# Kernel tuning notes

Measured on AMD Instinct MI355X. Metric: run time of the kernel, lower is better.

Reference implementation:

```python
import jax, jax.numpy as jnp
import numpy as np

B, N, K, C, H, W = 2, 8, 8, 256, 96, 96
CTX = C + K + 4 * K + 13  # 309
HID = 256
ALPHA = 0.3          # REFINE_EMA_ALPHA
TEMP = 1.0           # READOUT_TEMPERATURE
SIM_HIGH, SIM_LOW = 0.8, 0.3
A_KEEP, A_REFINE, A_REPLACE, A_SPAWN = 0, 1, 2, 3


def _l2norm(x, axis=-1, eps=1e-12):
    return x / jnp.maximum(jnp.linalg.norm(x, axis=axis, keepdims=True), eps)


def setup_inputs() -> dict:
    key = jax.random.key(0)
    ks = jax.random.split(key, 12)
    value = jax.random.normal(ks[0], (B, N, C, H, W), jnp.float32)
    frame_feat = jax.random.normal(ks[1], (B, C, H, W), jnp.float32)
    mask = jax.random.uniform(ks[2], (B, N, H, W), jnp.float32)
    proto = jax.random.normal(ks[3], (B, N, K, C), jnp.float32)
    age = jax.random.uniform(ks[4], (B, N, K), jnp.float32) * 10.0
    usage = jax.random.uniform(ks[5], (B, N, K), jnp.float32) * 5.0
    conf = jax.random.uniform(ks[6], (B, N, K), jnp.float32)
    valid = jax.random.randint(ks[7], (B, N, K), 0, 2).astype(bool)
    W1 = jax.random.normal(ks[8], (CTX, HID), jnp.float32) * 0.02
    b1 = jnp.zeros((HID,), jnp.float32)
    W2 = jax.random.normal(ks[9], (HID, 4), jnp.float32) * 0.02
    b2 = jnp.zeros((4,), jnp.float32)
    proto_gate = jnp.float32(1.0)
    frame_gate = jnp.float32(1.0)
    return dict(value=value, frame_feat=frame_feat, mask=mask, proto=proto,
                age=age, usage=usage, conf=conf, W1=W1, b1=b1, W2=W2, b2=b2,
                proto_gate=proto_gate, frame_gate=frame_gate, valid=valid)


def reference(value, frame_feat, mask, proto, age, usage, conf,
              W1, b1, W2, b2, proto_gate, frame_gate, valid):
    # ---- candidate prototype via masked pooling (PROTO_POOLING='mask') ----
    fv = value.reshape(B, N, C, H * W)                      # [B,N,C,HW]
    fm = mask.reshape(B, N, 1, H * W)                       # [B,N,1,HW]
    denom = jnp.maximum(fm.sum(-1), 1e-6)                   # [B,N,1]
    cand = (fv * fm).sum(-1) / denom                        # [B,N,C]
    mask_strength = fm.mean(-1)[..., 0]                     # [B,N]
    fallback = fv.mean(-1)
    cand = jnp.where((denom[..., 0] <= 1e-5)[..., None], fallback, cand)
    cand = _l2norm(cand)

    # ---- uncertainty features (prev_mask is None -> temporal term = 0) ----
    m = jnp.clip(mask, 1e-4, 1.0 - 1e-4)
    ent = -(m * jnp.log(m) + (1.0 - m) * jnp.log(1.0 - m))
    fg_prob = m.mean((-2, -1))
    fg_area = (m > 0.5).astype(jnp.float32).mean((-2, -1))
    gx = jnp.abs(m[..., 1:, :] - m[..., :-1, :]).mean((-2, -1))
    gy = jnp.abs(m[..., :, 1:] - m[..., :, :-1]).mean((-2, -1))
    unc = jnp.stack([ent.mean((-2, -1)), fg_prob, fg_area,
                     0.5 * (gx + gy), jnp.zeros_like(fg_prob)], -1)  # [B,N,5]

    # ---- context / similarity ----
    bank_n = _l2norm(proto)                                  # [B,N,K,C]
    sim = jnp.einsum('bnc,bnkc->bnk', cand, bank_n)
    sim = jnp.where(valid, sim, -1.0)
    g_t = jnp.broadcast_to(frame_feat.mean((2, 3))[:, None, :], (B, N, C))
    age_n = age / jnp.maximum(age.max(), 1.0)
    usage_n = usage / jnp.maximum(usage.max(), 1.0)
    bank_stats = jnp.stack([valid.astype(jnp.float32), age_n, usage_n, conf], -1)
    top2 = jax.lax.top_k(sim, 2)[0]
    t1, t2 = top2[..., 0], top2[..., 1]
    glob = jnp.stack([valid.astype(jnp.float32).mean(-1), age_n.max(-1),
                      usage_n.min(-1), conf.mean(-1), conf.max(-1)], -1)
    context = jnp.concatenate([g_t, sim, bank_stats.reshape(B, N, 4 * K),
                               jnp.stack([t1, t2, t1 - t2], -1), glob, unc], -1)
    logits = jax.nn.gelu(context @ W1 + b1, approximate=False) @ W2 + b2  # [B,N,4]

    any_valid = valid.any(-1)
    target_slot = jnp.where(any_valid, sim.argmax(-1), 0)
    max_sim = jnp.take_along_axis(sim, target_slot[..., None], -1)[..., 0]
    max_sim = jnp.where(any_valid, max_sim, -1.0)

    # ---- rule-based action selection ----
    action = jnp.where(~any_valid, A_SPAWN,
             jnp.where(max_sim >= SIM_HIGH, A_REFINE,
             jnp.where(max_sim >= SIM_LOW, A_KEEP, A_SPAWN)))

    # ---- victim / slot selection ----
    victim = (age_n + (1.0 - usage_n) + (1.0 - conf)).argmax(-1)
    first_empty = (~valid).argmax(-1)
    spawn_slot = jnp.where((~valid).any(-1), first_empty, victim)
    upd_slot = jnp.where(action == A_REFINE, target_slot, spawn_slot)

    # ---- policy-gated EMA scatter update of the bank ----
    onehot = jax.nn.one_hot(upd_slot, K, dtype=bool)                 # [B,N,K]
    refine_m = onehot & (action == A_REFINE)[..., None]
    write_m = onehot & (action == A_SPAWN)[..., None]
    refined = _l2norm((1.0 - ALPHA) * proto + ALPHA * cand[:, :, None, :])
    cand_b = jnp.broadcast_to(cand[:, :, None, :], proto.shape)
    proto_new = jnp.where(refine_m[..., None], refined,
                jnp.where(write_m[..., None], cand_b, proto))
    upd_m = refine_m | write_m
    age_new = jnp.where(upd_m, 0.0, age + 1.0)
    usage_new = usage + upd_m.astype(jnp.float32)
    conf_new = jnp.where(write_m, mask_strength[..., None],
               jnp.where(refine_m, jnp.maximum(conf, max_sim[..., None]), conf))
    valid_new = valid | write_m

    # ---- prototype-conditioned readout ----
    bank_nn = _l2norm(proto_new)                                      # [B,N,K,C]
    vn = value / jnp.maximum(jnp.linalg.norm(value, axis=2, keepdims=True), 1e-12)
    rsim = jnp.einsum('bnkc,bnchw->bnkhw', bank_nn, vn)
    rlog = jnp.where(valid_new[..., None, None], rsim / TEMP, -1e9)
    attn = jax.nn.softmax(rlog, axis=2)
    attn = attn * valid_new.any(-1)[..., None, None, None].astype(jnp.float32)
    proto_map = jnp.einsum('bnkhw,bnkc->bnchw', attn, proto_new)
    conditioned = value + proto_gate * proto_map + frame_gate * frame_feat[:, None]
    return conditioned
```

## Files before the change

### kernel.cpp

```cpp
#include <hip/hip_runtime.h>
#include <math.h>

constexpr int Bc = 2, Nc = 8, Kc = 8, Cc = 256, HWc = 96 * 96;
constexpr int BN = Bc * Nc;
constexpr int HW2 = HWc / 2;
constexpr float ALPHA = 0.3f;
constexpr float SIM_HIGH = 0.8f, SIM_LOW = 0.3f;
constexpr int TILES = 72;

__device__ __forceinline__ float wred_sum_all(float v) {
#pragma unroll
  for (int o = 32; o > 0; o >>= 1) v += __shfl_xor(v, o, 64);
  return v;
}
__device__ __forceinline__ float wred_sum(float v) {
#pragma unroll
  for (int o = 32; o > 0; o >>= 1) v += __shfl_down(v, o, 64);
  return v;
}
__device__ __forceinline__ float wred_max(float v) {
#pragma unroll
  for (int o = 32; o > 0; o >>= 1) v = fmaxf(v, __shfl_down(v, o, 64));
  return v;
}
__device__ __forceinline__ float bred_sum(float v, float* sc) {
  int lane = threadIdx.x & 63, wid = threadIdx.x >> 6;
  v = wred_sum(v);
  __syncthreads();
  if (lane == 0) sc[wid] = v;
  __syncthreads();
  return sc[0] + sc[1] + sc[2] + sc[3];
}
__device__ __forceinline__ float bred_max(float v, float* sc) {
  int lane = threadIdx.x & 63, wid = threadIdx.x >> 6;
  v = wred_max(v);
  __syncthreads();
  if (lane == 0) sc[wid] = v;
  __syncthreads();
  return fmaxf(fmaxf(sc[0], sc[1]), fmaxf(sc[2], sc[3]));
}

__device__ __forceinline__ float lane_bcast(float x, int c0) {
  return __int_as_float(__builtin_amdgcn_readlane(__float_as_int(x), c0));
}

__global__ __launch_bounds__(256) void k1_sums(const float* __restrict__ value,
                                               const float* __restrict__ mask,
                                               float* __restrict__ sum_v,
                                               float* __restrict__ sum_vm,
                                               float* __restrict__ msum) {
  const int bnc = blockIdx.x;
  const int bn = bnc >> 8;
  const int tid = threadIdx.x;
  const float4* v4 = (const float4*)(value + (size_t)bnc * HWc);
  const float4* m4 = (const float4*)(mask + (size_t)bn * HWc);
  float av = 0.f, avm = 0.f, am = 0.f;
#pragma unroll
  for (int i = 0; i < 9; ++i) {
    float4 v = v4[i * 256 + tid];
    float4 m = m4[i * 256 + tid];
    av += v.x + v.y + v.z + v.w;
    avm += v.x * m.x + v.y * m.y + v.z * m.z + v.w * m.w;
    am += (m.x + m.y) + (m.z + m.w);
  }
  __shared__ float sc[12];
  float rv = wred_sum(av);
  float rvm = wred_sum(avm);
  float rm = wred_sum(am);
  int lane = tid & 63, wid = tid >> 6;
  if (lane == 0) { sc[wid] = rv; sc[4 + wid] = rvm; sc[8 + wid] = rm; }
  __syncthreads();
  if (tid == 0) {
    sum_v[bnc] = sc[0] + sc[1] + sc[2] + sc[3];
    sum_vm[bnc] = sc[4] + sc[5] + sc[6] + sc[7];
    if ((bnc & 255) == 0)
      msum[bn] = sc[8] + sc[9] + sc[10] + sc[11];
  }
}

__global__ __launch_bounds__(256, 8) void k3_fused(
    const float* __restrict__ value, const float* __restrict__ frame,
    const float* __restrict__ mask_unused, const float* __restrict__ proto,
    const float* __restrict__ age, const float* __restrict__ usage,
    const float* __restrict__ conf, const int* __restrict__ valid,
    const float* __restrict__ sum_v, const float* __restrict__ sum_vm,
    const float* __restrict__ msum, const float* __restrict__ pgp,
    const float* __restrict__ fgp, float* __restrict__ out) {
  const int bn = blockIdx.x / TILES;
  const int tile = blockIdx.x % TILES;
  const int b = bn >> 3;
  const int tid = threadIdx.x;
  const int lane = tid & 63, w = tid >> 6;
  const int p2 = tile * 64 + lane;

  __shared__ union {
    struct { float cand[Cc]; float pn[Kc * Cc]; float sim[Kc]; } pre;
    float part[4 * 9 * 128];
  } u;
  __shared__ float sc[4];
  __shared__ float s_binv[Kc], s_vld[Kc];
  __shared__ int s_slot, s_ref, s_wr;

  float a = (tid < BN * Kc) ? age[tid] : -3e38f;
  float uu = (tid < BN * Kc) ? usage[tid] : -3e38f;
  const float age_den = fmaxf(bred_max(a, sc), 1.0f);
  const float usage_den = fmaxf(bred_max(uu, sc), 1.0f);

  const float denom = fmaxf(msum[bn], 1e-6f);

  const float sv = sum_v[bn * Cc + tid];
  const float svm = sum_vm[bn * Cc + tid];
  float cand = (denom <= 1e-5f) ? (sv * (1.0f / HWc)) : (svm / denom);
  const float css = bred_sum(cand * cand, sc);
  u.pre.cand[tid] = cand / fmaxf(sqrtf(css), 1e-12f);
  __syncthreads();

  const float4 c4 = ((const float4*)u.pre.cand)[lane];

  float4 p4k[2];
#pragma unroll
  for (int kk = 0; kk < 2; ++kk) {
    const int k = w + kk * 4;
    p4k[kk] = ((const float4*)(proto + ((size_t)bn * Kc + k) * Cc))[lane];
    const float4 p4 = p4k[kk];
    const float pss = wred_sum_all(p4.x * p4.x + p4.y * p4.y + p4.z * p4.z + p4.w * p4.w);
    const float pd  = wred_sum_all(p4.x * c4.x + p4.y * c4.y + p4.z * c4.z + p4.w * c4.w);
    if (lane == 0)
      u.pre.sim[k] = (valid[bn * Kc + k] != 0) ? (pd / fmaxf(sqrtf(pss), 1e-12f)) : -1.0f;
  }
  __syncthreads();

  if (tid == 0) {
    bool anyv = false;
    for (int k = 0; k < Kc; ++k) anyv = anyv || (valid[bn * Kc + k] != 0);
    int tslot = 0; float best = u.pre.sim[0];
    for (int k = 1; k < Kc; ++k)
      if (u.pre.sim[k] > best) { best = u.pre.sim[k]; tslot = k; }
    const float max_sim = anyv ? best : -1.0f;
    const int action = (!anyv) ? 3 : (max_sim >= SIM_HIGH ? 1 : (max_sim >= SIM_LOW ? 0 : 3));
    int victim = 0; float vb = -3e38f;
    for (int k = 0; k < Kc; ++k) {
      const float s = age[bn * Kc + k] / age_den + (1.f - usage[bn * Kc + k] / usage_den) +
                      (1.f - conf[bn * Kc + k]);
      if (s > vb) { vb = s; victim = k; }
    }
    int fe = 0; bool hasE = false;
    for (int k = 0; k < Kc; ++k)
      if (valid[bn * Kc + k] == 0) { fe = k; hasE = true; break; }
    const int spawn = hasE ? fe : victim;
    s_slot = (action == 1) ? tslot : spawn;
    s_ref = (action == 1);
    s_wr = (action == 3);
  }
  __syncthreads();

#pragma unroll
  for (int kk = 0; kk < 2; ++kk) {
    const int k = w + kk * 4;
    const float4 p4 = p4k[kk];
    float4 pn;
    if (k == s_slot && s_ref) {
      float4 t;
      t.x = (1.0f - ALPHA) * p4.x + ALPHA * c4.x;
      t.y = (1.0f - ALPHA) * p4.y + ALPHA * c4.y;
      t.z = (1.0f - ALPHA) * p4.z + ALPHA * c4.z;
      t.w = (1.0f - ALPHA) * p4.w + ALPHA * c4.w;
      const float tss = wred_sum_all(t.x * t.x + t.y * t.y + t.z * t.z + t.w * t.w);
      const float inv = 1.0f / fmaxf(sqrtf(tss), 1e-12f);
      pn.x = t.x * inv; pn.y = t.y * inv; pn.z = t.z * inv; pn.w = t.w * inv;
    } else if (k == s_slot && s_wr) {
      pn = c4;
    } else {
      pn = p4;
    }
    ((float4*)(u.pre.pn + k * Cc))[lane] = pn;
    const float bss = wred_sum_all(pn.x * pn.x + pn.y * pn.y + pn.z * pn.z + pn.w * pn.w);
    if (lane == 0) s_binv[k] = 1.0f / fmaxf(sqrtf(bss), 1e-12f);
  }
  if (tid < Kc)
    s_vld[tid] = ((valid[bn * Kc + tid] != 0) || (s_wr && tid == s_slot)) ? 1.0f : 0.0f;
  __syncthreads();

  float pnr[8], binv[8], vld[8];
#pragma unroll
  for (int k = 0; k < 8; ++k) {
    pnr[k] = u.pre.pn[k * Cc + w * 64 + lane];
    binv[k] = s_binv[k];
    vld[k] = s_vld[k];
  }
  __syncthreads();

  const float pg = pgp[0], fg = fgp[0];
  const float2* v2 = (const float2*)(value + (size_t)bn * Cc * HWc);
  const float2* f2 = (const float2*)(frame + (size_t)b * Cc * HWc);
  float2* o2 = (float2*)(out + (size_t)bn * Cc * HWc);

  float ss0 = 0.f, ss1 = 0.f;
  float d0[8], d1[8];
#pragma unroll
  for (int k = 0; k < 8; ++k) { d0[k] = 0.f; d1[k] = 0.f; }

#pragma unroll 8
  for (int c0 = 0; c0 < 64; ++c0) {
    const float2 v = v2[(size_t)(w * 64 + c0) * HW2 + p2];
    ss0 += v.x * v.x; ss1 += v.y * v.y;
#pragma unroll
    for (int k = 0; k < 8; ++k) {
      const float pk = lane_bcast(pnr[k], c0);
      d0[k] += pk * v.x;
      d1[k] += pk * v.y;
    }
  }

  float2* sp2 = (float2*)u.part;
#pragma unroll
  for (int k = 0; k < 8; ++k)
    sp2[(w * 9 + k) * 64 + lane] = make_float2(d0[k], d1[k]);
  sp2[(w * 9 + 8) * 64 + lane] = make_float2(ss0, ss1);
  __syncthreads();

  float a0[8], a1[8];
  {
    float dd0[9], dd1[9];
#pragma unroll
    for (int j = 0; j < 9; ++j) {
      const float2 t0 = sp2[(0 * 9 + j) * 64 + lane];
      const float2 t1 = sp2[(1 * 9 + j) * 64 + lane];
      const float2 t2 = sp2[(2 * 9 + j) * 64 + lane];
      const float2 t3 = sp2[(3 * 9 + j) * 64 + lane];
      dd0[j] = (t0.x + t1.x) + (t2.x + t3.x);
      dd1[j] = (t0.y + t1.y) + (t2.y + t3.y);
    }
    const float rn0 = 1.0f / fmaxf(sqrtf(dd0[8]), 1e-12f);
    const float rn1 = 1.0f / fmaxf(sqrtf(dd1[8]), 1e-12f);
    float m0 = -3e38f, m1 = -3e38f;
#pragma unroll
    for (int k = 0; k < 8; ++k) {
      const float scl = binv[k];
      dd0[k] *= scl * rn0;
      dd1[k] *= scl * rn1;
      if (vld[k] > 0.5f) { m0 = fmaxf(m0, dd0[k]); m1 = fmaxf(m1, dd1[k]); }
    }
    float sum0 = 0.f, sum1 = 0.f;
#pragma unroll
    for (int k = 0; k < 8; ++k) {
      a0[k] = (vld[k] > 0.5f) ? __expf(dd0[k] - m0) : 0.f;
      a1[k] = (vld[k] > 0.5f) ? __expf(dd1[k] - m1) : 0.f;
      sum0 += a0[k]; sum1 += a1[k];
    }
    const float i0 = (sum0 > 0.f) ? 1.0f / sum0 : 0.f;
    const float i1 = (sum1 > 0.f) ? 1.0f / sum1 : 0.f;
#pragma unroll
    for (int k = 0; k < 8; ++k) { a0[k] *= i0; a1[k] *= i1; }
  }

#pragma unroll 4
  for (int c0 = 0; c0 < 64; ++c0) {
    const size_t off = (size_t)(w * 64 + c0) * HW2 + p2;
    const float2 v = v2[off];
    const float2 f = f2[off];
    float pm0 = 0.f, pm1 = 0.f;
#pragma unroll
    for (int k = 0; k < 8; ++k) {
      const float pk = lane_bcast(pnr[k], c0);
      pm0 += a0[k] * pk;
      pm1 += a1[k] * pk;
    }
    float2 o;
    o.x = v.x + pg * pm0 + fg * f.x;
    o.y = v.y + pg * pm1 + fg * f.y;
    o2[off] = o;
  }
}

extern "C" void kernel_launch(void* const* d_in, const int* in_sizes, int n_in,
                              void* d_out, int out_size, void* d_ws, size_t ws_size,
                              hipStream_t stream) {
  const float* value = (const float*)d_in[0];
  const float* frame = (const float*)d_in[1];
  const float* mask  = (const float*)d_in[2];
  const float* proto = (const float*)d_in[3];
  const float* age   = (const float*)d_in[4];
  const float* usage = (const float*)d_in[5];
  const float* conf  = (const float*)d_in[6];
  const float* pg = (const float*)d_in[11];
  const float* fg = (const float*)d_in[12];
  const int* valid = (const int*)d_in[13];
  float* out = (float*)d_out;

  float* w = (float*)d_ws;
  float* sum_v  = w;
  float* sum_vm = w + 4096;
  float* msum   = w + 8192;

  hipLaunchKernelGGL(k1_sums, dim3(BN * Cc), dim3(256), 0, stream,
                     value, mask, sum_v, sum_vm, msum);
  hipLaunchKernelGGL(k3_fused, dim3(BN * TILES), dim3(256), 0, stream,
                     value, frame, mask, proto, age, usage, conf, valid,
                     sum_v, sum_vm, msum, pg, fg, out);
}
```

Baseline: 357.0 us.

## Split each wave across two channel halves and double tile count

Each wave now covers 32 pixel-pairs and splits its channel slice between two half-waves (even and odd channels), so the grid doubles from 72 to 144 tiles per (b,n). Channel-prototype broadcasts use __shfl instead of readlane, and partial dot products are combined across halves with a shfl_xor before the shared-memory reduction. The intent is more blocks and parallelism, shorter per-thread loops and smaller shared partials. The cost is that each block repeats the prototype-update preamble, shuffles go through LDS-style permutes rather than scalar readlane, and each memory access row is now 256 bytes rather than 512.

```diff
diff --git a/kernel.cpp b/kernel.cpp
--- a/kernel.cpp
+++ b/kernel.cpp
@@ -6,7 +6,7 @@
 constexpr int HW2 = HWc / 2;
 constexpr float ALPHA = 0.3f;
 constexpr float SIM_HIGH = 0.8f, SIM_LOW = 0.3f;
-constexpr int TILES = 72;
+constexpr int TILES = 144;
 
 __device__ __forceinline__ float wred_sum_all(float v) {
 #pragma unroll
@@ -38,10 +38,6 @@
   if (lane == 0) sc[wid] = v;
   __syncthreads();
   return fmaxf(fmaxf(sc[0], sc[1]), fmaxf(sc[2], sc[3]));
-}
-
-__device__ __forceinline__ float lane_bcast(float x, int c0) {
-  return __int_as_float(__builtin_amdgcn_readlane(__float_as_int(x), c0));
 }
 
 __global__ __launch_bounds__(256) void k1_sums(const float* __restrict__ value,
@@ -91,11 +87,14 @@
   const int b = bn >> 3;
   const int tid = threadIdx.x;
   const int lane = tid & 63, w = tid >> 6;
-  const int p2 = tile * 64 + lane;
+  const int h = lane >> 5;
+  const int p = lane & 31;
+  const int p2 = tile * 32 + p;
+  const int hbase = h << 5;
 
   __shared__ union {
     struct { float cand[Cc]; float pn[Kc * Cc]; float sim[Kc]; } pre;
-    float part[4 * 9 * 128];
+    float part[4 * 9 * 64];
   } u;
   __shared__ float sc[4];
   __shared__ float s_binv[Kc], s_vld[Kc];
@@ -181,10 +180,10 @@
     s_vld[tid] = ((valid[bn * Kc + tid] != 0) || (s_wr && tid == s_slot)) ? 1.0f : 0.0f;
   __syncthreads();
 
-  float pnr[8], binv[8], vld[8];
+  float rC[8], binv[8], vld[8];
 #pragma unroll
   for (int k = 0; k < 8; ++k) {
-    pnr[k] = u.pre.pn[k * Cc + w * 64 + lane];
+    rC[k] = u.pre.pn[k * Cc + w * 64 + 2 * p + h];
     binv[k] = s_binv[k];
     vld[k] = s_vld[k];
   }
@@ -201,22 +200,33 @@
   for (int k = 0; k < 8; ++k) { d0[k] = 0.f; d1[k] = 0.f; }
 
 #pragma unroll 8
-  for (int c0 = 0; c0 < 64; ++c0) {
-    const float2 v = v2[(size_t)(w * 64 + c0) * HW2 + p2];
+  for (int c0 = 0; c0 < 32; ++c0) {
+    const int c = w * 64 + 2 * c0 + h;
+    const float2 v = v2[(size_t)c * HW2 + p2];
     ss0 += v.x * v.x; ss1 += v.y * v.y;
 #pragma unroll
     for (int k = 0; k < 8; ++k) {
-      const float pk = lane_bcast(pnr[k], c0);
+      const float pk = __shfl(rC[k], hbase + c0, 64);
       d0[k] += pk * v.x;
       d1[k] += pk * v.y;
     }
   }
 
+#pragma unroll
+  for (int k = 0; k < 8; ++k) {
+    d0[k] += __shfl_xor(d0[k], 32, 64);
+    d1[k] += __shfl_xor(d1[k], 32, 64);
+  }
+  ss0 += __shfl_xor(ss0, 32, 64);
+  ss1 += __shfl_xor(ss1, 32, 64);
+
   float2* sp2 = (float2*)u.part;
-#pragma unroll
-  for (int k = 0; k < 8; ++k)
-    sp2[(w * 9 + k) * 64 + lane] = make_float2(d0[k], d1[k]);
-  sp2[(w * 9 + 8) * 64 + lane] = make_float2(ss0, ss1);
+  if (h == 0) {
+#pragma unroll
+    for (int k = 0; k < 8; ++k)
+      sp2[(w * 9 + k) * 32 + p] = make_float2(d0[k], d1[k]);
+    sp2[(w * 9 + 8) * 32 + p] = make_float2(ss0, ss1);
+  }
   __syncthreads();
 
   float a0[8], a1[8];
@@ -224,10 +234,10 @@
     float dd0[9], dd1[9];
 #pragma unroll
     for (int j = 0; j < 9; ++j) {
-      const float2 t0 = sp2[(0 * 9 + j) * 64 + lane];
-      const float2 t1 = sp2[(1 * 9 + j) * 64 + lane];
-      const float2 t2 = sp2[(2 * 9 + j) * 64 + lane];
-      const float2 t3 = sp2[(3 * 9 + j) * 64 + lane];
+      const float2 t0 = sp2[(0 * 9 + j) * 32 + p];
+      const float2 t1 = sp2[(1 * 9 + j) * 32 + p];
+      const float2 t2 = sp2[(2 * 9 + j) * 32 + p];
+      const float2 t3 = sp2[(3 * 9 + j) * 32 + p];
       dd0[j] = (t0.x + t1.x) + (t2.x + t3.x);
       dd1[j] = (t0.y + t1.y) + (t2.y + t3.y);
     }
@@ -255,14 +265,15 @@
   }
 
 #pragma unroll 4
-  for (int c0 = 0; c0 < 64; ++c0) {
-    const size_t off = (size_t)(w * 64 + c0) * HW2 + p2;
+  for (int c0 = 0; c0 < 32; ++c0) {
+    const int c = w * 64 + 2 * c0 + h;
+    const size_t off = (size_t)c * HW2 + p2;
     const float2 v = v2[off];
     const float2 f = f2[off];
     float pm0 = 0.f, pm1 = 0.f;
 #pragma unroll
     for (int k = 0; k < 8; ++k) {
-      const float pk = lane_bcast(pnr[k], c0);
+      const float pk = __shfl(rC[k], hbase + c0, 64);
       pm0 += a0[k] * pk;
       pm1 += a1[k] * pk;
     }
```

After: 371.9 us. 4.2% more time.
